# Performance work log

Hardware: AMD Instinct MI355X
Metric: run time of the kernel (lower is better)

The kernel has to match this reference:

```python
import jax, jax.numpy as jnp
import numpy as np

IMG, P, S, E, B = 224, 16, 8, 128, 64
N = (IMG - P) // S + 1          # patches per spatial dim (27)
L = N * N                       # num patches (729)
K = P * P                       # patch area (256)


def _flat_patch_idx():
    # flattened pixel index for each (patch, within-patch) element, shape [L, K]
    base = jnp.arange(N) * S            # top-left corner of each patch row/col
    off = jnp.arange(P)
    rows = base[:, None] + off[None, :]  # [N, P]
    hh = rows[:, None, :, None]          # [N,1,P,1]
    ww = rows[None, :, None, :]          # [1,N,1,P]
    return (hh * IMG + ww).reshape(L, K)  # row-major over patch positions, i*P+j within patch (matches torch Unfold)


def setup_inputs() -> dict:
    key = jax.random.key(0)
    k = jax.random.split(key, 5)
    x = jax.random.normal(k[0], (B, 3, IMG, IMG), dtype=jnp.float32)
    W_enc = jax.random.normal(k[1], (3, E, K), dtype=jnp.float32) * 0.02
    b_enc = jax.random.normal(k[2], (3, E), dtype=jnp.float32) * 0.02
    W_dec = jax.random.normal(k[3], (3, K, E), dtype=jnp.float32) * 0.02
    b_dec = jax.random.normal(k[4], (3, K), dtype=jnp.float32) * 0.02
    return {"x": x, "W_enc": W_enc, "b_enc": b_enc, "W_dec": W_dec, "b_dec": b_dec}


def reference(x, W_enc, b_enc, W_dec, b_dec):
    flat = _flat_patch_idx()                         # [L, K] int indices, static
    Bn = x.shape[0]
    # unfold: gather overlapping patches -> [B, 3, L, K]
    patches = x.reshape(Bn, 3, IMG * IMG)[:, :, flat]
    # per-channel linear encode: [B,3,L,E]
    emb = jnp.einsum('bclk,cek->bcle', patches, W_enc) + b_enc[:, None, :]
    # per-channel linear decode: [B,3,L,K]
    rec = jnp.einsum('bcle,cke->bclk', emb, W_dec) + b_dec[:, None, :]
    # fold: overlap-add scatter back to image
    fi = flat.reshape(-1)
    out = jnp.zeros((Bn, 3, IMG * IMG), x.dtype).at[:, :, fi].add(rec.reshape(Bn, 3, L * K))
    # normalization = fold(unfold(ones)) = per-pixel overlap count
    count = jnp.zeros((IMG * IMG,), x.dtype).at[fi].add(jnp.ones((L * K,), x.dtype))
    return (out / count).reshape(Bn, 3, IMG, IMG)
```

## Files before the change

### kernel.cpp

```cpp
#include <hip/hip_runtime.h>

#define IMG   224
#define IMG2  (IMG*IMG)
#define NN    27
#define KK    256
#define EE    128
#define SCOLS 232
#define RSTR  136

typedef float f32x4 __attribute__((ext_vector_type(4)));
typedef short s16x8 __attribute__((ext_vector_type(8)));

__device__ __forceinline__ unsigned short f2bf(float f) {
    unsigned int u = __float_as_uint(f);
    u = (u + 0x7fffu + ((u >> 16) & 1u)) >> 16;
    return (unsigned short)u;
}
__device__ __forceinline__ float bf2f(unsigned short u) {
    return __uint_as_float((unsigned int)u << 16);
}
__device__ __forceinline__ uint2 pack4(f32x4 r) {
    uint2 u;
    asm("v_cvt_pk_bf16_f32 %0, %1, %2" : "=v"(u.x) : "v"(r.x), "v"(r.y));
    asm("v_cvt_pk_bf16_f32 %0, %1, %2" : "=v"(u.y) : "v"(r.z), "v"(r.w));
    return u;
}

__global__ void pack_M(const float* __restrict__ W_enc, const float* __restrict__ W_dec,
                       const float* __restrict__ b_enc, const float* __restrict__ b_dec,
                       unsigned short* __restrict__ APK, float* __restrict__ v) {
    int k = blockIdx.x, c = blockIdx.y, j = threadIdx.x;
    const float* wd = W_dec + ((size_t)c*KK + k)*EE;
    const float* we = W_enc + (size_t)c*EE*KK + j;
    float acc = 0.f;
    #pragma unroll 8
    for (int e = 0; e < EE; ++e) acc = fmaf(wd[e], we[(size_t)e*KK], acc);
    int kf = k >> 4, kr = k & 15, jb = j >> 5, g = (j >> 3) & 3, i = j & 7;
    APK[(size_t)c*65536 + (((kf*8 + jb)*64) + g*16 + kr)*8 + i] = f2bf(acc);

    __shared__ float pv[128];
    if (j < EE) pv[j] = wd[j] * b_enc[c*EE + j];
    __syncthreads();
    for (int off = 64; off > 0; off >>= 1) {
        if (j < off) pv[j] += pv[j + off];
        __syncthreads();
    }
    if (j == 0) v[c*KK + k] = pv[0] + b_dec[c*KK + k];
}

__global__ __launch_bounds__(512, 4)
void patch_ae_loop(const float* __restrict__ x, const unsigned short* __restrict__ APK,
                   const float* __restrict__ v, float* __restrict__ out) {
    const int hid = blockIdx.x;
    const int lid = (hid & 7)*96 + (hid >> 3);
    const int q   = lid & 3;
    const int t2  = lid >> 2;
    const int c   = t2 % 3;
    const int b   = t2 / 3;
    const int s0  = 7*q;

    const int tid  = threadIdx.x;
    const int lane = tid & 63, wave = tid >> 6;

    __shared__ __align__(16) unsigned short ring[32*SCOLS];
    __shared__ __align__(16) unsigned short rec[2][30][RSTR];
    __shared__ __align__(16) float vsh[256];

    if (tid < 256) vsh[tid] = v[c*256 + tid];
    if (tid < RSTR) {
        rec[0][0][tid] = 0; rec[0][28][tid] = 0;
        rec[1][0][tid] = 0; rec[1][28][tid] = 0;
    }

    const int prow   = wave >> 2;
    const int kq     = wave & 3;
    const int kfbase = prow*8 + kq*2;
    const int g = lane >> 4, lr = lane & 15;
    const int jx0 = (g & 1)*8;
    const int c1 = (lr <= 10) ? (128 + 8*lr) : 208;
    const int rowoff = prow ? -8 : 0;

    const int kfu = __builtin_amdgcn_readfirstlane(kfbase);
    const char* abase = (const char*)(APK + (size_t)c*65536) + (size_t)kfu*8192;
    const int v0a = lane*16,       v0b = v0a + 4096;
    const int v1a = v0a + 8192,    v1b = v0a + 12288;

#define ALD(VAR, VOFF, OFFSTR)                                      \
    asm volatile("global_load_dwordx4 %0, %1, %2 offset:" OFFSTR    \
                 : "=v"(VAR) : "v"(VOFF), "s"(abase));

    s16x8 a0_0,a0_1,a0_2,a0_3,a0_4,a0_5,a0_6,a0_7;
    s16x8 a1_0,a1_1,a1_2,a1_3,a1_4,a1_5,a1_6,a1_7;
    ALD(a0_0, v0a, "0")  ALD(a0_1, v0a, "1024") ALD(a0_2, v0a, "2048") ALD(a0_3, v0a, "3072")
    ALD(a0_4, v0b, "0")  ALD(a0_5, v0b, "1024") ALD(a0_6, v0b, "2048") ALD(a0_7, v0b, "3072")
    ALD(a1_0, v1a, "0")  ALD(a1_1, v1a, "1024") ALD(a1_2, v1a, "2048") ALD(a1_3, v1a, "3072")
    ALD(a1_4, v1b, "0")  ALD(a1_5, v1b, "1024") ALD(a1_6, v1b, "2048") ALD(a1_7, v1b, "3072")
#undef ALD

    const float* xb = x + (size_t)(b*3 + c)*IMG2;

    #pragma unroll
    for (int it = 0; it < 2; ++it) {
        int ci = tid + it*512;
        if (ci < 672) {
            int r  = ci / 28, cc = ci - (ci/28)*28;
            int ar = 8*s0 - 8 + r;
            int yr = ar < 0 ? 0 : (ar > 223 ? 223 : ar);
            const float4* src = (const float4*)(xb + (size_t)yr*IMG + cc*8);
            float4 lo = src[0], hi = src[1];
            uint2 u0 = pack4((f32x4){lo.x, lo.y, lo.z, lo.w});
            uint2 u1 = pack4((f32x4){hi.x, hi.y, hi.z, hi.w});
            *((uint4*)&ring[(ar & 31)*SCOLS + cc*8]) = make_uint4(u0.x, u0.y, u1.x, u1.y);
        }
    }
    __syncthreads();
    asm volatile("s_waitcnt vmcnt(0)");
    __builtin_amdgcn_sched_barrier(0);

    const int rr  = tid / 28;
    const int cc2 = tid - 28*(tid/28);

    const int eq  = tid % 28, ery = tid / 28;
    const int ev1 = (eq < 27), ev0 = (eq > 0);
    const int ero = ery*16;

#define MFMA2(AF, B0, B1, F)                                                             \
        acc[F][0] = __builtin_amdgcn_mfma_f32_16x16x32_bf16(AF, B0, acc[F][0], 0, 0, 0); \
        acc[F][1] = __builtin_amdgcn_mfma_f32_16x16x32_bf16(AF, B1, acc[F][1], 0, 0, 0);

#define MSTEP(JB, A0, A1)                                                            \
        {                                                                            \
            const int jy = 2*(JB) + (g >> 1);                                        \
            const unsigned short* srow = &ring[((rowb + jy) & 31)*SCOLS + jx0];      \
            s16x8 bf0 = *((const s16x8*)&srow[8*lr]);                                \
            s16x8 bf1 = *((const s16x8*)&srow[c1]);                                  \
            __builtin_amdgcn_s_setprio(1);                                           \
            MFMA2(A0, bf0, bf1, 0) MFMA2(A1, bf0, bf1, 1)                            \
            __builtin_amdgcn_s_setprio(0);                                           \
        }

    #pragma unroll 1
    for (int s = s0; s < s0 + 7; ++s) {
        f32x4 ga0, ga1;
        if (tid < 224) {
            int yr = 8*(s+2) + rr; if (yr > 223) yr = 223;
            int voffx = yr*(IMG*4) + cc2*32;
            asm volatile("global_load_dwordx4 %0, %1, %2"           : "=v"(ga0) : "v"(voffx), "s"(xb));
            asm volatile("global_load_dwordx4 %0, %1, %2 offset:16" : "=v"(ga1) : "v"(voffx), "s"(xb));
        }

        f32x4 acc[2][2];
        #pragma unroll
        for (int f = 0; f < 2; ++f)
            #pragma unroll
            for (int pf = 0; pf < 2; ++pf)
                acc[f][pf] = (f32x4){0.f, 0.f, 0.f, 0.f};
        const int rowb = 8*s + rowoff;
        MSTEP(0, a0_0, a1_0)
        MSTEP(1, a0_1, a1_1)
        MSTEP(2, a0_2, a1_2)
        MSTEP(3, a0_3, a1_3)
        MSTEP(4, a0_4, a1_4)
        MSTEP(5, a0_5, a1_5)
        MSTEP(6, a0_6, a1_6)
        MSTEP(7, a0_7, a1_7)

        #pragma unroll
        for (int f = 0; f < 2; ++f) {
            int klocal = kq*32 + f*16 + g*4;
            f32x4 bias = *((const f32x4*)&vsh[prow*128 + klocal]);
            #pragma unroll
            for (int pf = 0; pf < 2; ++pf) {
                f32x4 r = acc[f][pf] + bias;
                int pidx = pf*16 + lr + 1;
                if (pidx >= 28) pidx = 29;
                *((uint2*)&rec[prow][pidx][klocal]) = pack4(r);
            }
        }
        __syncthreads();

        if (tid < 224) {
            asm volatile("s_waitcnt vmcnt(0)");
            __builtin_amdgcn_sched_barrier(0);
            uint2 u0 = pack4(ga0);
            uint2 u1 = pack4(ga1);
            int ar2 = 8*(s+2) + rr;
            *((uint4*)&ring[(ar2 & 31)*SCOLS + cc2*8]) = make_uint4(u0.x, u0.y, u1.x, u1.y);
        }

        if (tid < 224) {
            const int h0 = (s < 27);
            const int h1 = (s > 0);
            const int shift = (ev0 & ev1) + (h0 & h1);
            const float inv = __int_as_float(0x3f800000 - (shift << 23));
            float sum[8];
            #pragma unroll
            for (int d = 0; d < 8; ++d) sum[d] = 0.f;
            if (h0) {
                s16x8 rrv = *((const s16x8*)&rec[0][eq+1][ero]);
                s16x8 llv = *((const s16x8*)&rec[0][eq][ero + 8]);
                #pragma unroll
                for (int d = 0; d < 8; ++d)
                    sum[d] += bf2f((unsigned short)rrv[d]) + bf2f((unsigned short)llv[d]);
            }
            if (h1) {
                s16x8 rrv = *((const s16x8*)&rec[1][eq+1][ero]);
                s16x8 llv = *((const s16x8*)&rec[1][eq][ero + 8]);
                #pragma unroll
                for (int d = 0; d < 8; ++d)
                    sum[d] += bf2f((unsigned short)rrv[d]) + bf2f((unsigned short)llv[d]);
            }
            float* orow = out + (size_t)(b*3 + c)*IMG2 + (size_t)(8*s + ery)*IMG + 8*eq;
            f32x4 o0 = {sum[0]*inv, sum[1]*inv, sum[2]*inv, sum[3]*inv};
            f32x4 o1 = {sum[4]*inv, sum[5]*inv, sum[6]*inv, sum[7]*inv};
            *((f32x4*)orow)       = o0;
            *((f32x4*)(orow + 4)) = o1;
        }
        __syncthreads();
    }
#undef MSTEP
#undef MFMA2
}

extern "C" void kernel_launch(void* const* d_in, const int* in_sizes, int n_in,
                              void* d_out, int out_size, void* d_ws, size_t ws_size,
                              hipStream_t stream) {
    (void)in_sizes; (void)n_in; (void)out_size; (void)ws_size;
    const float* x     = (const float*)d_in[0];
    const float* W_enc = (const float*)d_in[1];
    const float* b_enc = (const float*)d_in[2];
    const float* W_dec = (const float*)d_in[3];
    const float* b_dec = (const float*)d_in[4];
    float* out = (float*)d_out;

    float*          v   = (float*)d_ws;
    unsigned short* APK = (unsigned short*)((char*)d_ws + 4096);

    pack_M<<<dim3(KK, 3), 256, 0, stream>>>(W_enc, W_dec, b_enc, b_dec, APK, v);
    patch_ae_loop<<<dim3(768), 512, 0, stream>>>(x, APK, v, out);
}
```

Measured before the change: 41.01 us.

## Spread per-step load and epilogue over 448 threads; pack_M computes two rows per block

The main loop now uses 448 threads instead of 224 for the next-row prefetch and the overlap-add epilogue. Each thread loads one float4 instead of two and writes four output floats instead of eight, halving the serial work per thread. The prefetched-row conversion and ring store is moved after the epilogue so the global load has more time to arrive. pack_M now computes two k rows per block, reusing each W_enc load across both and halving its grid size.

```diff
diff --git a/kernel.cpp b/kernel.cpp
--- a/kernel.cpp
+++ b/kernel.cpp
@@ -10,6 +10,7 @@
 
 typedef float f32x4 __attribute__((ext_vector_type(4)));
 typedef short s16x8 __attribute__((ext_vector_type(8)));
+typedef short s16x4 __attribute__((ext_vector_type(4)));
 
 __device__ __forceinline__ unsigned short f2bf(float f) {
     unsigned int u = __float_as_uint(f);
@@ -29,23 +30,35 @@
 __global__ void pack_M(const float* __restrict__ W_enc, const float* __restrict__ W_dec,
                        const float* __restrict__ b_enc, const float* __restrict__ b_dec,
                        unsigned short* __restrict__ APK, float* __restrict__ v) {
-    int k = blockIdx.x, c = blockIdx.y, j = threadIdx.x;
-    const float* wd = W_dec + ((size_t)c*KK + k)*EE;
-    const float* we = W_enc + (size_t)c*EE*KK + j;
-    float acc = 0.f;
+    const int k0 = blockIdx.x*2, c = blockIdx.y, j = threadIdx.x;
+    const float* wd0 = W_dec + ((size_t)c*KK + k0)*EE;
+    const float* wd1 = wd0 + EE;
+    const float* we  = W_enc + (size_t)c*EE*KK + j;
+    float a0 = 0.f, a1 = 0.f;
     #pragma unroll 8
-    for (int e = 0; e < EE; ++e) acc = fmaf(wd[e], we[(size_t)e*KK], acc);
-    int kf = k >> 4, kr = k & 15, jb = j >> 5, g = (j >> 3) & 3, i = j & 7;
-    APK[(size_t)c*65536 + (((kf*8 + jb)*64) + g*16 + kr)*8 + i] = f2bf(acc);
-
-    __shared__ float pv[128];
-    if (j < EE) pv[j] = wd[j] * b_enc[c*EE + j];
+    for (int e = 0; e < EE; ++e) {
+        float wv = we[(size_t)e*KK];
+        a0 = fmaf(wd0[e], wv, a0);
+        a1 = fmaf(wd1[e], wv, a1);
+    }
+    const int jb = j >> 5, g = (j >> 3) & 3, i = j & 7;
+    {
+        int kf = k0 >> 4, kr = k0 & 15;
+        APK[(size_t)c*65536 + (((kf*8 + jb)*64) + g*16 + kr)*8 + i] = f2bf(a0);
+        kf = (k0+1) >> 4; kr = (k0+1) & 15;
+        APK[(size_t)c*65536 + (((kf*8 + jb)*64) + g*16 + kr)*8 + i] = f2bf(a1);
+    }
+
+    __shared__ float pv[256];
+    const float* be = b_enc + c*EE;
+    pv[j] = (j < EE) ? wd0[j]*be[j] : wd1[j-EE]*be[j-EE];
     __syncthreads();
     for (int off = 64; off > 0; off >>= 1) {
-        if (j < off) pv[j] += pv[j + off];
+        if ((j & 127) < off) pv[j] += pv[j + off];
         __syncthreads();
     }
-    if (j == 0) v[c*KK + k] = pv[0] + b_dec[c*KK + k];
+    if (j == 0)   v[c*KK + k0]     = pv[0]   + b_dec[c*KK + k0];
+    if (j == 128) v[c*KK + k0 + 1] = pv[128] + b_dec[c*KK + k0 + 1];
 }
 
 __global__ __launch_bounds__(512, 4)
@@ -117,12 +130,14 @@
     asm volatile("s_waitcnt vmcnt(0)");
     __builtin_amdgcn_sched_barrier(0);
 
-    const int rr  = tid / 28;
-    const int cc2 = tid - 28*(tid/28);
-
-    const int eq  = tid % 28, ery = tid / 28;
-    const int ev1 = (eq < 27), ev0 = (eq > 0);
-    const int ero = ery*16;
+    const int sr  = tid / 56;
+    const int sc4 = tid - 56*(tid/56);
+
+    const int em   = tid % 56, ery = tid / 56;
+    const int eq   = em >> 1, ehh = em & 1;
+    const int ev1  = (eq < 27), ev0 = (eq > 0);
+    const int kl1  = ery*16 + 4*ehh;
+    const int kl0  = kl1 + 8;
 
 #define MFMA2(AF, B0, B1, F)                                                             \
         acc[F][0] = __builtin_amdgcn_mfma_f32_16x16x32_bf16(AF, B0, acc[F][0], 0, 0, 0); \
@@ -141,12 +156,11 @@
 
     #pragma unroll 1
     for (int s = s0; s < s0 + 7; ++s) {
-        f32x4 ga0, ga1;
-        if (tid < 224) {
-            int yr = 8*(s+2) + rr; if (yr > 223) yr = 223;
-            int voffx = yr*(IMG*4) + cc2*32;
-            asm volatile("global_load_dwordx4 %0, %1, %2"           : "=v"(ga0) : "v"(voffx), "s"(xb));
-            asm volatile("global_load_dwordx4 %0, %1, %2 offset:16" : "=v"(ga1) : "v"(voffx), "s"(xb));
+        f32x4 ga0;
+        if (tid < 448) {
+            int yr = 8*(s+2) + sr; if (yr > 223) yr = 223;
+            int voffx = yr*(IMG*4) + sc4*16;
+            asm volatile("global_load_dwordx4 %0, %1, %2" : "=v"(ga0) : "v"(voffx), "s"(xb));
         }
 
         f32x4 acc[2][2];
@@ -179,42 +193,39 @@
         }
         __syncthreads();
 
-        if (tid < 224) {
-            asm volatile("s_waitcnt vmcnt(0)");
-            __builtin_amdgcn_sched_barrier(0);
-            uint2 u0 = pack4(ga0);
-            uint2 u1 = pack4(ga1);
-            int ar2 = 8*(s+2) + rr;
-            *((uint4*)&ring[(ar2 & 31)*SCOLS + cc2*8]) = make_uint4(u0.x, u0.y, u1.x, u1.y);
-        }
-
-        if (tid < 224) {
+        if (tid < 448) {
             const int h0 = (s < 27);
             const int h1 = (s > 0);
             const int shift = (ev0 & ev1) + (h0 & h1);
             const float inv = __int_as_float(0x3f800000 - (shift << 23));
-            float sum[8];
+            float sum[4];
             #pragma unroll
-            for (int d = 0; d < 8; ++d) sum[d] = 0.f;
+            for (int d = 0; d < 4; ++d) sum[d] = 0.f;
             if (h0) {
-                s16x8 rrv = *((const s16x8*)&rec[0][eq+1][ero]);
-                s16x8 llv = *((const s16x8*)&rec[0][eq][ero + 8]);
+                s16x4 rrv = *((const s16x4*)&rec[0][eq+1][kl1]);
+                s16x4 llv = *((const s16x4*)&rec[0][eq][kl0]);
                 #pragma unroll
-                for (int d = 0; d < 8; ++d)
+                for (int d = 0; d < 4; ++d)
                     sum[d] += bf2f((unsigned short)rrv[d]) + bf2f((unsigned short)llv[d]);
             }
             if (h1) {
-                s16x8 rrv = *((const s16x8*)&rec[1][eq+1][ero]);
-                s16x8 llv = *((const s16x8*)&rec[1][eq][ero + 8]);
+                s16x4 rrv = *((const s16x4*)&rec[1][eq+1][kl1]);
+                s16x4 llv = *((const s16x4*)&rec[1][eq][kl0]);
                 #pragma unroll
-                for (int d = 0; d < 8; ++d)
+                for (int d = 0; d < 4; ++d)
                     sum[d] += bf2f((unsigned short)rrv[d]) + bf2f((unsigned short)llv[d]);
             }
-            float* orow = out + (size_t)(b*3 + c)*IMG2 + (size_t)(8*s + ery)*IMG + 8*eq;
-            f32x4 o0 = {sum[0]*inv, sum[1]*inv, sum[2]*inv, sum[3]*inv};
-            f32x4 o1 = {sum[4]*inv, sum[5]*inv, sum[6]*inv, sum[7]*inv};
-            *((f32x4*)orow)       = o0;
-            *((f32x4*)(orow + 4)) = o1;
+            float* orow = out + (size_t)(b*3 + c)*IMG2 + (size_t)(8*s + ery)*IMG + 4*em;
+            f32x4 o = {sum[0]*inv, sum[1]*inv, sum[2]*inv, sum[3]*inv};
+            *((f32x4*)orow) = o;
+        }
+
+        if (tid < 448) {
+            asm volatile("s_waitcnt vmcnt(0)");
+            __builtin_amdgcn_sched_barrier(0);
+            uint2 u0 = pack4(ga0);
+            int ar2 = 8*(s+2) + sr;
+            *((uint2*)&ring[(ar2 & 31)*SCOLS + sc4*4]) = u0;
         }
         __syncthreads();
     }
@@ -236,6 +247,6 @@
     float*          v   = (float*)d_ws;
     unsigned short* APK = (unsigned short*)((char*)d_ws + 4096);
 
-    pack_M<<<dim3(KK, 3), 256, 0, stream>>>(W_enc, W_dec, b_enc, b_dec, APK, v);
+    pack_M<<<dim3(KK/2, 3), 256, 0, stream>>>(W_enc, W_dec, b_enc, b_dec, APK, v);
     patch_ae_loop<<<dim3(768), 512, 0, stream>>>(x, APK, v, out);
 }
```

Result: no change. 40.42 us (-1.5%).
